# Kernel optimization log

Measured on AMD Instinct MI355X. Metric: run time of the kernel, lower is better.

The kernel has to match this reference:

```python
import jax, jax.numpy as jnp
import numpy as np

N = 10000        # nodes
E = 160000       # edges (avg degree 16)
MUL = 16         # multiplicity of each irrep in node features: '16x0e + 16x1o'
DIM_IN = 4 * MUL # 16 scalars + 16 vectors(3) = 64
DIM_SH = 4       # '1x0e + 1x1o' spherical harmonics
EMB = 18         # 2*4 (type embeds) + 10 (distance embed)
HID = 256
WNUM = 4 * MUL * MUL  # 4 tensor-product paths, 16x16 weights each


def setup_inputs() -> dict:
    key = jax.random.key(0)
    ks = jax.random.split(key, 8)
    node_features = jax.random.normal(ks[0], (N, DIM_IN), jnp.float32)
    edge_src = jax.random.randint(ks[1], (E,), 0, N, dtype=jnp.int32)
    edge_dst = jax.random.randint(ks[2], (E,), 0, N, dtype=jnp.int32)
    edge_attr = jax.random.normal(ks[3], (E, DIM_SH), jnp.float32)
    edge_embedding = jax.random.normal(ks[4], (E, EMB), jnp.float32)
    W1 = jax.random.normal(ks[5], (EMB, HID), jnp.float32) / np.sqrt(EMB)
    b1 = jnp.zeros((HID,), jnp.float32)
    W2 = jax.random.normal(ks[6], (HID, WNUM), jnp.float32) / np.sqrt(HID)
    b2 = jnp.zeros((WNUM,), jnp.float32)
    return dict(node_features=node_features, edge_attr=edge_attr,
                edge_embedding=edge_embedding, W1=W1, b1=b1, W2=W2, b2=b2,
                edge_src=edge_src, edge_dst=edge_dst)


def reference(node_features, edge_attr, edge_embedding, W1, b1, W2, b2, edge_src, edge_dst):
    # ---- edge MLP generates per-edge tensor-product weights ----
    h = jax.nn.silu(edge_embedding @ W1 + b1)          # [E, HID]
    w = (h @ W2 + b2).reshape(E, 4, MUL, MUL)          # [E, 4, 16, 16]
    w_ss, w_vv, w_sv, w_vs = w[:, 0], w[:, 1], w[:, 2], w[:, 3]

    # ---- gather source node features, split into irreps ----
    x = node_features[edge_src]                        # [E, 64]
    s = x[:, :MUL]                                     # [E, 16]   16x0e
    v = x[:, MUL:].reshape(E, MUL, 3)                  # [E, 16, 3] 16x1o
    y0 = edge_attr[:, 0]                               # [E]       1x0e sh
    y1 = edge_attr[:, 1:4]                             # [E, 3]    1x1o sh

    # ---- weighted Clebsch-Gordan tensor product (lmax=1 paths) ----
    inv_sqrt3 = np.float32(1.0 / np.sqrt(3.0))         # w3j(1,1,0), w3j(0,1,1), w3j(1,0,1)
    c_s = np.float32(np.sqrt(1.0 / (2 * MUL)))         # path norm: 2 paths, fan_in MUL each, out dim 1
    c_v = np.float32(np.sqrt(3.0 / (2 * MUL)))         # path norm: 2 paths, fan_in MUL each, out dim 3
    # 0e x 0e -> 0e  and  1o x 1o -> 0e
    out_s = c_s * (jnp.einsum('eij,e,ei->ej', w_ss, y0, s)
                   + inv_sqrt3 * jnp.einsum('eij,ea,eia->ej', w_vv, y1, v))   # [E, 16]
    # 0e x 1o -> 1o  and  1o x 0e -> 1o
    out_v = (c_v * inv_sqrt3) * (jnp.einsum('eij,ei,ea->eja', w_sv, s, y1)
                                 + jnp.einsum('eij,eia,e->eja', w_vs, v, y0))  # [E, 16, 3]

    edge_features = jnp.concatenate([out_s, out_v.reshape(E, 3 * MUL)], axis=1)  # [E, 64]

    # ---- scatter-reduce to destination nodes, normalized by sqrt(avg degree) ----
    num_neighbors = E / float(N)
    out = jax.ops.segment_sum(edge_features, edge_dst, num_segments=N)
    return out / np.float32(np.sqrt(num_neighbors))
```

## Files before the change

### kernel.cpp

```cpp
#include <hip/hip_runtime.h>
#include <math.h>


typedef __attribute__((ext_vector_type(8))) short s8v;
typedef __attribute__((ext_vector_type(4))) float f4v;
typedef unsigned short ushort_t;
typedef unsigned int uint_t;

#define NTHR 256
#define TE 64

__device__ __forceinline__ ushort_t f2bf(float x) {
    uint_t u = __float_as_uint(x);
    u += 0x7fffu + ((u >> 16) & 1u);
    return (ushort_t)(u >> 16);
}

__global__ void conv_w2(const float* __restrict__ W2, ushort_t* __restrict__ W2bf) {
    int idx = blockIdx.x * 256 + threadIdx.x;
    int n  = idx & 1023;
    int k4 = (idx >> 10) << 2;
    uint_t lo = (uint_t)f2bf(W2[(size_t)(k4 + 0) * 1024 + n]) |
                ((uint_t)f2bf(W2[(size_t)(k4 + 1) * 1024 + n]) << 16);
    uint_t hi = (uint_t)f2bf(W2[(size_t)(k4 + 2) * 1024 + n]) |
                ((uint_t)f2bf(W2[(size_t)(k4 + 3) * 1024 + n]) << 16);
    ((uint2*)W2bf)[(n * 256 + k4) >> 2] = make_uint2(lo, hi);
}

__global__ void hist_kernel(const int* __restrict__ edst, int* __restrict__ counts, int E) {
    int i = blockIdx.x * 256 + threadIdx.x;
    if (i < E) atomicAdd(&counts[edst[i]], 1);
}

__global__ __launch_bounds__(1024)
void scan_kernel(const int* __restrict__ counts, int* __restrict__ offsets, int N) {
    __shared__ int sdata[1024];
    const int t = threadIdx.x;
    const int C = (N + 1023) / 1024;
    const int lo = t * C;
    const int hi = min(lo + C, N);
    int sum = 0;
    for (int i = lo; i < hi; ++i) sum += counts[i];
    sdata[t] = sum;
    __syncthreads();
    for (int s = 1; s < 1024; s <<= 1) {
        int v = (t >= s) ? sdata[t - s] : 0;
        __syncthreads();
        sdata[t] += v;
        __syncthreads();
    }
    int run = sdata[t] - sum;
    for (int i = lo; i < hi; ++i) { offsets[i] = run; run += counts[i]; }
    if (t == 1023) offsets[N] = run;
}

__global__ void fill_kernel(const int* __restrict__ edst,
                            const int* __restrict__ offsets,
                            int* __restrict__ cursor,
                            int* __restrict__ elist, int E) {
    int i = blockIdx.x * 256 + threadIdx.x;
    if (i < E) {
        int d = edst[i];
        int pos = offsets[d] + atomicAdd(&cursor[d], 1);
        elist[pos] = i;
    }
}

__global__ __launch_bounds__(256)
void gather_kernel(const float* __restrict__ F,
                   const int* __restrict__ offsets,
                   const int* __restrict__ elist,
                   float* __restrict__ out, int N) {
    const int lane = threadIdx.x & 63;
    const int node = (blockIdx.x * 256 + threadIdx.x) >> 6;
    if (node >= N) return;
    const int base = offsets[node];
    const int end  = offsets[node + 1];
    float acc = 0.f;
    for (int j0 = base; j0 < end; j0 += 64) {
        const int rem = min(64, end - j0);
        int myeid = (lane < rem) ? elist[j0 + lane] : 0;
        int j = 0;
        for (; j + 4 <= rem; j += 4) {
            const int a0 = __shfl(myeid, j    );
            const int a1 = __shfl(myeid, j + 1);
            const int a2 = __shfl(myeid, j + 2);
            const int a3 = __shfl(myeid, j + 3);
            const float r0 = F[(size_t)a0 * 64 + lane];
            const float r1 = F[(size_t)a1 * 64 + lane];
            const float r2 = F[(size_t)a2 * 64 + lane];
            const float r3 = F[(size_t)a3 * 64 + lane];
            acc += (r0 + r1) + (r2 + r3);
        }
        for (; j < rem; ++j) {
            const int a = __shfl(myeid, j);
            acc += F[(size_t)a * 64 + lane];
        }
    }
    out[(size_t)node * 64 + lane] = acc;
}

__global__ __launch_bounds__(NTHR, 2)
void nequip_mfma(const float* __restrict__ nodef,
                 const float* __restrict__ eattr,
                 const float* __restrict__ eemb,
                 const float* __restrict__ W1,
                 const float* __restrict__ b1,
                 const ushort_t* __restrict__ W2bf,
                 const float* __restrict__ b2,
                 const int* __restrict__ esrc,
                 float* __restrict__ F,
                 int E, float CC)
{
    __shared__ __align__(16) ushort_t sAu[TE * 256];
    __shared__ __align__(16) float sB2[1024];
    __shared__ __align__(16) float sEmb[TE * 18];
    __shared__ __align__(16) float sCss[16 * 64];
    __shared__ __align__(16) float sCvv[16 * 64];
    __shared__ __align__(16) float sCsv[16 * 64];
    __shared__ __align__(16) float sCvs[48 * 64];
    __shared__ __align__(16) float sAttrT[4 * 64];
    __shared__ __align__(16) float resSS[64 * 16];
    __shared__ __align__(16) float resSV[64 * 16];

    const int t  = threadIdx.x;
    const int e0 = blockIdx.x * TE;

    ((float4*)sB2)[t] = ((const float4*)b2)[t];
    for (int idx = t; idx < TE * 18; idx += NTHR) {
        size_t g = (size_t)e0 * 18 + idx;
        sEmb[idx] = (g < (size_t)E * 18) ? eemb[g] : 0.f;
    }
    if (t < TE) {
        int ge = e0 + t;
        float4 a = make_float4(0.f, 0.f, 0.f, 0.f);
        if (ge < E) a = *(const float4*)(eattr + (size_t)ge * 4);
        sAttrT[0 * 64 + t] = a.x; sAttrT[1 * 64 + t] = a.y;
        sAttrT[2 * 64 + t] = a.z; sAttrT[3 * 64 + t] = a.w;
    }
    {
        const int e = t >> 2, iq = t & 3;
        const int ge = e0 + e;
        const bool ok = ge < E;
        float y0 = 0.f, y1x = 0.f, y1y = 0.f, y1z = 0.f;
        int src = 0;
        if (ok) {
            float4 a = *(const float4*)(eattr + (size_t)ge * 4);
            y0 = a.x; y1x = a.y; y1y = a.z; y1z = a.w;
            src = esrc[ge];
        }
        const float* xp = nodef + (size_t)src * 64;
        float4 z = make_float4(0.f, 0.f, 0.f, 0.f);
        float4 sv = ok ? *(const float4*)(xp + iq * 4) : z;
        float4 v0 = ok ? *(const float4*)(xp + 16 + iq * 12) : z;
        float4 v1 = ok ? *(const float4*)(xp + 16 + iq * 12 + 4) : z;
        float4 v2 = ok ? *(const float4*)(xp + 16 + iq * 12 + 8) : z;
        const float K3 = CC * 0.57735026918962576f;
        float sarr[4] = { sv.x, sv.y, sv.z, sv.w };
        float varr[12] = { v0.x, v0.y, v0.z, v0.w, v1.x, v1.y, v1.z, v1.w,
                           v2.x, v2.y, v2.z, v2.w };
        #pragma unroll
        for (int j = 0; j < 4; ++j) {
            const int i = iq * 4 + j;
            const float s  = sarr[j];
            const float vx = varr[j * 3 + 0], vy = varr[j * 3 + 1], vz = varr[j * 3 + 2];
            sCss[i * 64 + e] = CC * y0 * s;
            sCvv[i * 64 + e] = K3 * (y1x * vx + y1y * vy + y1z * vz);
            sCsv[i * 64 + e] = CC * s;
            sCvs[(i * 3 + 0) * 64 + e] = CC * y0 * vx;
            sCvs[(i * 3 + 1) * 64 + e] = CC * y0 * vy;
            sCvs[(i * 3 + 2) * 64 + e] = CC * y0 * vz;
        }
    }
    __syncthreads();

    {
        const int p = t & 127;
        const int ehalf = t >> 7;
        const int n0 = 2 * p;
        float w1a[18], w1b[18];
        #pragma unroll
        for (int m = 0; m < 18; ++m) {
            float2 wv = *(const float2*)(W1 + m * 256 + n0);
            w1a[m] = wv.x; w1b[m] = wv.y;
        }
        const float2 bv = *(const float2*)(b1 + n0);
        const int kk = p >> 4;
        const int lhi = 16 * ((p >> 2) & 3);
        const int wsub = p & 3;
        uint_t* sA32 = (uint_t*)sAu;
        for (int er = 0; er < 32; ++er) {
            const int e = ehalf * 32 + er;
            float a0 = bv.x, a1 = bv.y;
            const float* ep = sEmb + e * 18;
            #pragma unroll
            for (int m = 0; m < 18; ++m) {
                const float em = ep[m];
                a0 = fmaf(em, w1a[m], a0);
                a1 = fmaf(em, w1b[m], a1);
            }
            a0 = a0 / (1.f + __expf(-a0));
            a1 = a1 / (1.f + __expf(-a1));
            const uint_t pk = (uint_t)f2bf(a0) | ((uint_t)f2bf(a1) << 16);
            const int lane_sw = ((e & 15) + lhi) ^ kk;
            sA32[(((e >> 4) * 8 + kk) * 64 + lane_sw) * 4 + wsub] = pk;
        }
    }
    __syncthreads();

    const int lane = t & 63;
    const int slab = t >> 6;
    const int jj   = lane & 15;
    const int q4   = lane >> 4;

    const ushort_t* Bl = W2bf + (size_t)jj * 256 + q4 * 8;

    float pS[4][4] = {{0.f}};
    float pV[3][4][4] = {{{0.f}}};

    if (slab < 3) {
        const float* C = (slab == 0) ? sCss : (slab == 1) ? sCvv : sCsv;
        #pragma unroll 1
        for (int g = 0; g < 8; ++g) {
            const int nb0 = slab * 256 + (2 * g) * 16;
            const int nb1 = nb0 + 16;
            f4v accA[4], accB[4];
            {
                const float bz0 = sB2[nb0 + jj];
                const float bz1 = sB2[nb1 + jj];
                #pragma unroll
                for (int mt = 0; mt < 4; ++mt) {
                    f4v zA; zA[0] = bz0; zA[1] = bz0; zA[2] = bz0; zA[3] = bz0;
                    f4v zB; zB[0] = bz1; zB[1] = bz1; zB[2] = bz1; zB[3] = bz1;
                    accA[mt] = zA; accB[mt] = zB;
                }
            }
            #pragma unroll
            for (int kk = 0; kk < 8; ++kk) {
                const s8v b0 = *(const s8v*)(Bl + (size_t)nb0 * 256 + kk * 32);
                const s8v b1 = *(const s8v*)(Bl + (size_t)nb1 * 256 + kk * 32);
                #pragma unroll
                for (int mt = 0; mt < 4; ++mt) {
                    const s8v a = *(const s8v*)(sAu + ((mt * 8 + kk) * 64 + (lane ^ kk)) * 8);
                    accA[mt] = __builtin_amdgcn_mfma_f32_16x16x32_bf16(a, b0, accA[mt], 0, 0, 0);
                    accB[mt] = __builtin_amdgcn_mfma_f32_16x16x32_bf16(a, b1, accB[mt], 0, 0, 0);
                }
            }
            const int i0 = 2 * g, i1 = 2 * g + 1;
            #pragma unroll
            for (int mt = 0; mt < 4; ++mt) {
                const int ebase = mt * 16 + q4 * 4;
                const float4 c0 = *(const float4*)(C + i0 * 64 + ebase);
                const float4 c1 = *(const float4*)(C + i1 * 64 + ebase);
                pS[mt][0] += c0.x * accA[mt][0] + c1.x * accB[mt][0];
                pS[mt][1] += c0.y * accA[mt][1] + c1.y * accB[mt][1];
                pS[mt][2] += c0.z * accA[mt][2] + c1.z * accB[mt][2];
                pS[mt][3] += c0.w * accA[mt][3] + c1.w * accB[mt][3];
            }
        }
        if (slab == 0) {
            #pragma unroll
            for (int mt = 0; mt < 4; ++mt)
                #pragma unroll
                for (int q = 0; q < 4; ++q)
                    resSS[(mt * 16 + q4 * 4 + q) * 16 + jj] = pS[mt][q];
        } else if (slab == 2) {
            #pragma unroll
            for (int mt = 0; mt < 4; ++mt)
                #pragma unroll
                for (int q = 0; q < 4; ++q)
                    resSV[(mt * 16 + q4 * 4 + q) * 16 + jj] = pS[mt][q];
        }
    } else {
        #pragma unroll 1
        for (int ti = 0; ti < 16; ++ti) {
            const int nb = 3 * 256 + ti * 16;
            f4v acc[4];
            {
                const float bz = sB2[nb + jj];
                #pragma unroll
                for (int mt = 0; mt < 4; ++mt) {
                    f4v z; z[0] = bz; z[1] = bz; z[2] = bz; z[3] = bz;
                    acc[mt] = z;
                }
            }
            #pragma unroll
            for (int kk = 0; kk < 8; ++kk) {
                const s8v b = *(const s8v*)(Bl + (size_t)nb * 256 + kk * 32);
                #pragma unroll
                for (int mt = 0; mt < 4; ++mt) {
                    const s8v a = *(const s8v*)(sAu + ((mt * 8 + kk) * 64 + (lane ^ kk)) * 8);
                    acc[mt] = __builtin_amdgcn_mfma_f32_16x16x32_bf16(a, b, acc[mt], 0, 0, 0);
                }
            }
            #pragma unroll
            for (int mt = 0; mt < 4; ++mt) {
                const int ebase = mt * 16 + q4 * 4;
                #pragma unroll
                for (int a = 0; a < 3; ++a) {
                    const float4 c = *(const float4*)(sCvs + (ti * 3 + a) * 64 + ebase);
                    pV[a][mt][0] = fmaf(c.x, acc[mt][0], pV[a][mt][0]);
                    pV[a][mt][1] = fmaf(c.y, acc[mt][1], pV[a][mt][1]);
                    pV[a][mt][2] = fmaf(c.z, acc[mt][2], pV[a][mt][2]);
                    pV[a][mt][3] = fmaf(c.w, acc[mt][3], pV[a][mt][3]);
                }
            }
        }
    }
    __syncthreads();

    if (slab == 1) {
        #pragma unroll
        for (int mt = 0; mt < 4; ++mt) {
            #pragma unroll
            for (int q = 0; q < 4; ++q) {
                const int e = mt * 16 + q4 * 4 + q;
                const int ge = e0 + e;
                if (ge < E) F[(size_t)ge * 64 + jj] = resSS[e * 16 + jj] + pS[mt][q];
            }
        }
    } else if (slab == 3) {
        #pragma unroll
        for (int mt = 0; mt < 4; ++mt) {
            #pragma unroll
            for (int q = 0; q < 4; ++q) {
                const int e = mt * 16 + q4 * 4 + q;
                const int ge = e0 + e;
                const float sv = resSV[e * 16 + jj];
                if (ge < E) {
                    #pragma unroll
                    for (int a = 0; a < 3; ++a)
                        F[(size_t)ge * 64 + 16 + jj * 3 + a] =
                            fmaf(sAttrT[(1 + a) * 64 + e], sv, pV[a][mt][q]);
                }
            }
        }
    }
}

extern "C" void kernel_launch(void* const* d_in, const int* in_sizes, int n_in,
                              void* d_out, int out_size, void* d_ws, size_t ws_size,
                              hipStream_t stream)
{
    const float* node_features = (const float*)d_in[0];
    const float* edge_attr     = (const float*)d_in[1];
    const float* edge_emb      = (const float*)d_in[2];
    const float* W1            = (const float*)d_in[3];
    const float* b1            = (const float*)d_in[4];
    const float* W2            = (const float*)d_in[5];
    const float* b2            = (const float*)d_in[6];
    const int*   edge_src      = (const int*)d_in[7];
    const int*   edge_dst      = (const int*)d_in[8];
    float*       out           = (float*)d_out;

    const int E = in_sizes[7];
    const int N = out_size / 64;
    const float num_neigh = (float)E / (float)N;
    const float CC = 0.17677669529663689f / sqrtf(num_neigh);

    char* ws = (char*)d_ws;
    size_t off = 0;
    auto alloc = [&](size_t bytes) { char* p = ws + off; off = (off + bytes + 255) & ~(size_t)255; return p; };
    ushort_t* W2bf   = (ushort_t*)alloc((size_t)1024 * 256 * 2);
    int*      counts = (int*)alloc((size_t)N * 4);
    int*      offs   = (int*)alloc((size_t)(N + 1) * 4);
    int*      cursor = (int*)alloc((size_t)N * 4);
    int*      elist  = (int*)alloc((size_t)E * 4);
    float*    F      = (float*)alloc((size_t)E * 64 * 4);
    (void)ws_size;

    hipMemsetAsync(counts, 0, (size_t)N * 4, stream);
    hipMemsetAsync(cursor, 0, (size_t)N * 4, stream);

    conv_w2<<<256, 256, 0, stream>>>(W2, W2bf);
    hist_kernel<<<(E + 255) / 256, 256, 0, stream>>>(edge_dst, counts, E);
    scan_kernel<<<1, 1024, 0, stream>>>(counts, offs, N);
    fill_kernel<<<(E + 255) / 256, 256, 0, stream>>>(edge_dst, offs, cursor, elist, E);

    const int blocks = (E + TE - 1) / TE;
    nequip_mfma<<<blocks, NTHR, 0, stream>>>(
        node_features, edge_attr, edge_emb, W1, b1, W2bf, b2,
        edge_src, F, E, CC);

    gather_kernel<<<(N + 3) / 4, 256, 0, stream>>>(F, offs, elist, out, N);
}
```

Baseline: 366.3 us.

## Store edge features as bf16, merge prep kernels, and regroup MFMA loops

The per-edge feature buffer F is now written as bf16 and converted back to fp32 in the gather kernel. This halves the intermediate write and the random-read traffic. The W2 conversion and the histogram kernels are merged into one launch, and the two memsets become one. The scalar slabs now compute four output groups per iteration instead of two. The vector slab is split into two halves over edge tiles, with two groups per iteration. These changes trade register pressure and bf16 rounding of the summed features for less memory traffic and fewer launches.

```diff
diff --git a/kernel.cpp b/kernel.cpp
--- a/kernel.cpp
+++ b/kernel.cpp
@@ -15,21 +15,25 @@
     u += 0x7fffu + ((u >> 16) & 1u);
     return (ushort_t)(u >> 16);
 }
-
-__global__ void conv_w2(const float* __restrict__ W2, ushort_t* __restrict__ W2bf) {
-    int idx = blockIdx.x * 256 + threadIdx.x;
-    int n  = idx & 1023;
-    int k4 = (idx >> 10) << 2;
-    uint_t lo = (uint_t)f2bf(W2[(size_t)(k4 + 0) * 1024 + n]) |
-                ((uint_t)f2bf(W2[(size_t)(k4 + 1) * 1024 + n]) << 16);
-    uint_t hi = (uint_t)f2bf(W2[(size_t)(k4 + 2) * 1024 + n]) |
-                ((uint_t)f2bf(W2[(size_t)(k4 + 3) * 1024 + n]) << 16);
-    ((uint2*)W2bf)[(n * 256 + k4) >> 2] = make_uint2(lo, hi);
-}
-
-__global__ void hist_kernel(const int* __restrict__ edst, int* __restrict__ counts, int E) {
-    int i = blockIdx.x * 256 + threadIdx.x;
-    if (i < E) atomicAdd(&counts[edst[i]], 1);
+__device__ __forceinline__ float bf2f(ushort_t v) {
+    return __uint_as_float((uint_t)v << 16);
+}
+
+__global__ void prep_kernel(const float* __restrict__ W2, ushort_t* __restrict__ W2bf,
+                            const int* __restrict__ edst, int* __restrict__ counts, int E) {
+    if (blockIdx.x < 256) {
+        int idx = blockIdx.x * 256 + threadIdx.x;
+        int n  = idx & 1023;
+        int k4 = (idx >> 10) << 2;
+        uint_t lo = (uint_t)f2bf(W2[(size_t)(k4 + 0) * 1024 + n]) |
+                    ((uint_t)f2bf(W2[(size_t)(k4 + 1) * 1024 + n]) << 16);
+        uint_t hi = (uint_t)f2bf(W2[(size_t)(k4 + 2) * 1024 + n]) |
+                    ((uint_t)f2bf(W2[(size_t)(k4 + 3) * 1024 + n]) << 16);
+        ((uint2*)W2bf)[(n * 256 + k4) >> 2] = make_uint2(lo, hi);
+    } else {
+        int i = (blockIdx.x - 256) * 256 + threadIdx.x;
+        if (i < E) atomicAdd(&counts[edst[i]], 1);
+    }
 }
 
 __global__ __launch_bounds__(1024)
@@ -67,7 +71,7 @@
 }
 
 __global__ __launch_bounds__(256)
-void gather_kernel(const float* __restrict__ F,
+void gather_kernel(const ushort_t* __restrict__ F,
                    const int* __restrict__ offsets,
                    const int* __restrict__ elist,
                    float* __restrict__ out, int N) {
@@ -86,15 +90,15 @@
             const int a1 = __shfl(myeid, j + 1);
             const int a2 = __shfl(myeid, j + 2);
             const int a3 = __shfl(myeid, j + 3);
-            const float r0 = F[(size_t)a0 * 64 + lane];
-            const float r1 = F[(size_t)a1 * 64 + lane];
-            const float r2 = F[(size_t)a2 * 64 + lane];
-            const float r3 = F[(size_t)a3 * 64 + lane];
+            const float r0 = bf2f(F[(size_t)a0 * 64 + lane]);
+            const float r1 = bf2f(F[(size_t)a1 * 64 + lane]);
+            const float r2 = bf2f(F[(size_t)a2 * 64 + lane]);
+            const float r3 = bf2f(F[(size_t)a3 * 64 + lane]);
             acc += (r0 + r1) + (r2 + r3);
         }
         for (; j < rem; ++j) {
             const int a = __shfl(myeid, j);
-            acc += F[(size_t)a * 64 + lane];
+            acc += bf2f(F[(size_t)a * 64 + lane]);
         }
     }
     out[(size_t)node * 64 + lane] = acc;
@@ -109,7 +113,7 @@
                  const ushort_t* __restrict__ W2bf,
                  const float* __restrict__ b2,
                  const int* __restrict__ esrc,
-                 float* __restrict__ F,
+                 ushort_t* __restrict__ F,
                  int E, float CC)
 {
     __shared__ __align__(16) ushort_t sAu[TE * 256];
@@ -221,41 +225,43 @@
     if (slab < 3) {
         const float* C = (slab == 0) ? sCss : (slab == 1) ? sCvv : sCsv;
         #pragma unroll 1
-        for (int g = 0; g < 8; ++g) {
-            const int nb0 = slab * 256 + (2 * g) * 16;
-            const int nb1 = nb0 + 16;
-            f4v accA[4], accB[4];
-            {
-                const float bz0 = sB2[nb0 + jj];
-                const float bz1 = sB2[nb1 + jj];
+        for (int g = 0; g < 4; ++g) {
+            f4v acc[4][4];
+            #pragma unroll
+            for (int gi = 0; gi < 4; ++gi) {
+                const float bz = sB2[slab * 256 + (4 * g + gi) * 16 + jj];
                 #pragma unroll
                 for (int mt = 0; mt < 4; ++mt) {
-                    f4v zA; zA[0] = bz0; zA[1] = bz0; zA[2] = bz0; zA[3] = bz0;
-                    f4v zB; zB[0] = bz1; zB[1] = bz1; zB[2] = bz1; zB[3] = bz1;
-                    accA[mt] = zA; accB[mt] = zB;
+                    f4v z; z[0] = bz; z[1] = bz; z[2] = bz; z[3] = bz;
+                    acc[gi][mt] = z;
                 }
             }
             #pragma unroll
             for (int kk = 0; kk < 8; ++kk) {
-                const s8v b0 = *(const s8v*)(Bl + (size_t)nb0 * 256 + kk * 32);
-                const s8v b1 = *(const s8v*)(Bl + (size_t)nb1 * 256 + kk * 32);
+                s8v b[4];
+                #pragma unroll
+                for (int gi = 0; gi < 4; ++gi)
+                    b[gi] = *(const s8v*)(Bl + (size_t)(slab * 256 + (4 * g + gi) * 16) * 256 + kk * 32);
                 #pragma unroll
                 for (int mt = 0; mt < 4; ++mt) {
                     const s8v a = *(const s8v*)(sAu + ((mt * 8 + kk) * 64 + (lane ^ kk)) * 8);
-                    accA[mt] = __builtin_amdgcn_mfma_f32_16x16x32_bf16(a, b0, accA[mt], 0, 0, 0);
-                    accB[mt] = __builtin_amdgcn_mfma_f32_16x16x32_bf16(a, b1, accB[mt], 0, 0, 0);
-                }
-            }
-            const int i0 = 2 * g, i1 = 2 * g + 1;
-            #pragma unroll
-            for (int mt = 0; mt < 4; ++mt) {
-                const int ebase = mt * 16 + q4 * 4;
-                const float4 c0 = *(const float4*)(C + i0 * 64 + ebase);
-                const float4 c1 = *(const float4*)(C + i1 * 64 + ebase);
-                pS[mt][0] += c0.x * accA[mt][0] + c1.x * accB[mt][0];
-                pS[mt][1] += c0.y * accA[mt][1] + c1.y * accB[mt][1];
-                pS[mt][2] += c0.z * accA[mt][2] + c1.z * accB[mt][2];
-                pS[mt][3] += c0.w * accA[mt][3] + c1.w * accB[mt][3];
+                    #pragma unroll
+                    for (int gi = 0; gi < 4; ++gi)
+                        acc[gi][mt] = __builtin_amdgcn_mfma_f32_16x16x32_bf16(a, b[gi], acc[gi][mt], 0, 0, 0);
+                }
+            }
+            #pragma unroll
+            for (int gi = 0; gi < 4; ++gi) {
+                const int i = 4 * g + gi;
+                #pragma unroll
+                for (int mt = 0; mt < 4; ++mt) {
+                    const int ebase = mt * 16 + q4 * 4;
+                    const float4 c = *(const float4*)(C + i * 64 + ebase);
+                    pS[mt][0] = fmaf(c.x, acc[gi][mt][0], pS[mt][0]);
+                    pS[mt][1] = fmaf(c.y, acc[gi][mt][1], pS[mt][1]);
+                    pS[mt][2] = fmaf(c.z, acc[gi][mt][2], pS[mt][2]);
+                    pS[mt][3] = fmaf(c.w, acc[gi][mt][3], pS[mt][3]);
+                }
             }
         }
         if (slab == 0) {
@@ -273,36 +279,48 @@
         }
     } else {
         #pragma unroll 1
-        for (int ti = 0; ti < 16; ++ti) {
-            const int nb = 3 * 256 + ti * 16;
-            f4v acc[4];
-            {
-                const float bz = sB2[nb + jj];
-                #pragma unroll
-                for (int mt = 0; mt < 4; ++mt) {
-                    f4v z; z[0] = bz; z[1] = bz; z[2] = bz; z[3] = bz;
-                    acc[mt] = z;
-                }
-            }
-            #pragma unroll
-            for (int kk = 0; kk < 8; ++kk) {
-                const s8v b = *(const s8v*)(Bl + (size_t)nb * 256 + kk * 32);
-                #pragma unroll
-                for (int mt = 0; mt < 4; ++mt) {
-                    const s8v a = *(const s8v*)(sAu + ((mt * 8 + kk) * 64 + (lane ^ kk)) * 8);
-                    acc[mt] = __builtin_amdgcn_mfma_f32_16x16x32_bf16(a, b, acc[mt], 0, 0, 0);
-                }
-            }
-            #pragma unroll
-            for (int mt = 0; mt < 4; ++mt) {
-                const int ebase = mt * 16 + q4 * 4;
-                #pragma unroll
-                for (int a = 0; a < 3; ++a) {
-                    const float4 c = *(const float4*)(sCvs + (ti * 3 + a) * 64 + ebase);
-                    pV[a][mt][0] = fmaf(c.x, acc[mt][0], pV[a][mt][0]);
-                    pV[a][mt][1] = fmaf(c.y, acc[mt][1], pV[a][mt][1]);
-                    pV[a][mt][2] = fmaf(c.z, acc[mt][2], pV[a][mt][2]);
-                    pV[a][mt][3] = fmaf(c.w, acc[mt][3], pV[a][mt][3]);
+        for (int half = 0; half < 2; ++half) {
+            #pragma unroll 1
+            for (int g = 0; g < 8; ++g) {
+                const int i0 = 2 * g, i1 = 2 * g + 1;
+                const int nb0 = 3 * 256 + i0 * 16;
+                const int nb1 = nb0 + 16;
+                f4v acc0[2], acc1[2];
+                {
+                    const float bz0 = sB2[nb0 + jj];
+                    const float bz1 = sB2[nb1 + jj];
+                    #pragma unroll
+                    for (int mt = 0; mt < 2; ++mt) {
+                        f4v z0; z0[0] = bz0; z0[1] = bz0; z0[2] = bz0; z0[3] = bz0;
+                        f4v z1; z1[0] = bz1; z1[1] = bz1; z1[2] = bz1; z1[3] = bz1;
+                        acc0[mt] = z0; acc1[mt] = z1;
+                    }
+                }
+                #pragma unroll
+                for (int kk = 0; kk < 8; ++kk) {
+                    const s8v b0 = *(const s8v*)(Bl + (size_t)nb0 * 256 + kk * 32);
+                    const s8v b1 = *(const s8v*)(Bl + (size_t)nb1 * 256 + kk * 32);
+                    #pragma unroll
+                    for (int mt = 0; mt < 2; ++mt) {
+                        const int mtg = half * 2 + mt;
+                        const s8v a = *(const s8v*)(sAu + ((mtg * 8 + kk) * 64 + (lane ^ kk)) * 8);
+                        acc0[mt] = __builtin_amdgcn_mfma_f32_16x16x32_bf16(a, b0, acc0[mt], 0, 0, 0);
+                        acc1[mt] = __builtin_amdgcn_mfma_f32_16x16x32_bf16(a, b1, acc1[mt], 0, 0, 0);
+                    }
+                }
+                #pragma unroll
+                for (int mt = 0; mt < 2; ++mt) {
+                    const int mtg = half * 2 + mt;
+                    const int ebase = mtg * 16 + q4 * 4;
+                    #pragma unroll
+                    for (int a = 0; a < 3; ++a) {
+                        const float4 c0 = *(const float4*)(sCvs + (i0 * 3 + a) * 64 + ebase);
+                        const float4 c1 = *(const float4*)(sCvs + (i1 * 3 + a) * 64 + ebase);
+                        pV[a][mtg][0] += c0.x * acc0[mt][0] + c1.x * acc1[mt][0];
+                        pV[a][mtg][1] += c0.y * acc0[mt][1] + c1.y * acc1[mt][1];
+                        pV[a][mtg][2] += c0.z * acc0[mt][2] + c1.z * acc1[mt][2];
+                        pV[a][mtg][3] += c0.w * acc0[mt][3] + c1.w * acc1[mt][3];
+                    }
                 }
             }
         }
@@ -316,7 +334,7 @@
             for (int q = 0; q < 4; ++q) {
                 const int e = mt * 16 + q4 * 4 + q;
                 const int ge = e0 + e;
-                if (ge < E) F[(size_t)ge * 64 + jj] = resSS[e * 16 + jj] + pS[mt][q];
+                if (ge < E) F[(size_t)ge * 64 + jj] = f2bf(resSS[e * 16 + jj] + pS[mt][q]);
             }
         }
     } else if (slab == 3) {
@@ -331,7 +349,7 @@
                     #pragma unroll
                     for (int a = 0; a < 3; ++a)
                         F[(size_t)ge * 64 + 16 + jj * 3 + a] =
-                            fmaf(sAttrT[(1 + a) * 64 + e], sv, pV[a][mt][q]);
+                            f2bf(fmaf(sAttrT[(1 + a) * 64 + e], sv, pV[a][mt][q]));
                 }
             }
         }
@@ -362,20 +380,19 @@
     size_t off = 0;
     auto alloc = [&](size_t bytes) { char* p = ws + off; off = (off + bytes + 255) & ~(size_t)255; return p; };
     ushort_t* W2bf   = (ushort_t*)alloc((size_t)1024 * 256 * 2);
-    int*      counts = (int*)alloc((size_t)N * 4);
+    int*      counts = (int*)alloc((size_t)2 * N * 4);
+    int*      cursor = counts + N;
     int*      offs   = (int*)alloc((size_t)(N + 1) * 4);
-    int*      cursor = (int*)alloc((size_t)N * 4);
     int*      elist  = (int*)alloc((size_t)E * 4);
-    float*    F      = (float*)alloc((size_t)E * 64 * 4);
+    ushort_t* F      = (ushort_t*)alloc((size_t)E * 64 * 2);
     (void)ws_size;
 
-    hipMemsetAsync(counts, 0, (size_t)N * 4, stream);
-    hipMemsetAsync(cursor, 0, (size_t)N * 4, stream);
-
-    conv_w2<<<256, 256, 0, stream>>>(W2, W2bf);
-    hist_kernel<<<(E + 255) / 256, 256, 0, stream>>>(edge_dst, counts, E);
+    hipMemsetAsync(counts, 0, (size_t)2 * N * 4, stream);
+
+    const int histBlocks = (E + 255) / 256;
+    prep_kernel<<<256 + histBlocks, 256, 0, stream>>>(W2, W2bf, edge_dst, counts, E);
     scan_kernel<<<1, 1024, 0, stream>>>(counts, offs, N);
-    fill_kernel<<<(E + 255) / 256, 256, 0, stream>>>(edge_dst, offs, cursor, elist, E);
+    fill_kernel<<<histBlocks, 256, 0, stream>>>(edge_dst, offs, cursor, elist, E);
 
     const int blocks = (E + TE - 1) / TE;
     nequip_mfma<<<blocks, NTHR, 0, stream>>>(
```

New measurement: 389.1 us. 6.2% more time.
